# Optimization experiments

Measured on AMD Instinct MI355X. Metric: run time of the kernel, lower is better.

Reference implementation:

```python
import jax, jax.numpy as jnp
import numpy as np

UNITS = 64
NUM_LEVELS = 4
ORDER = 4  # order=-1 defaults to num_levels
NUM_FEATURES = 64  # 63 input features + 1 time channel
LEN_TENSORS = NUM_LEVELS * (NUM_LEVELS + 1) // 2  # 10


def setup_inputs() -> dict:
    key = jax.random.key(0)
    k1, k2 = jax.random.split(key)
    X = jax.random.normal(k1, (32, 2048, 63), dtype=jnp.float32)
    # learned low-rank kernel [num_features, len_tensors, units]; small scale keeps
    # higher-level signature products numerically tame
    kernel = jax.random.normal(k2, (NUM_FEATURES, LEN_TENSORS, UNITS), dtype=jnp.float32) * 0.02
    return {"X": X, "kernel": kernel}


def _ecumsum(x):
    # exclusive cumulative sum along time axis (axis=1), forward direction
    return jnp.cumsum(x, axis=1) - x


def reference(X, kernel):
    B, T, _ = X.shape
    # add_time=True: linear time channel in [-1, 1]
    t = jnp.arange(T, dtype=X.dtype) * (2.0 / (T - 1.0)) - 1.0
    time = jnp.broadcast_to(t[None, :, None], (B, T, 1))
    Xa = jnp.concatenate([time, X], axis=-1)  # [B, T, F]
    # low-rank projection: [B, T, len_tensors, units]
    M = jnp.einsum('btf,fku->btku', Xa, kernel)
    # difference=True: forward increments, zero-padded at t=0
    M = jnp.concatenate([jnp.zeros_like(M[:, :1]), M[:, 1:] - M[:, :-1]], axis=1)

    # level 1
    out = jnp.sum(M[..., 0, :], axis=1)  # [B, units]

    k = 1
    for m in range(1, NUM_LEVELS):
        R = [M[..., k, :]]  # list of [B, T, units]
        k += 1
        for i in range(1, m + 1):
            d = min(i + 1, ORDER)
            A = sum(R)
            Mk = M[..., k, :]
            R_next = [Mk * _ecumsum(A)]
            for j in range(1, d):
                R_next.append(Mk * R[j - 1] / jnp.asarray(j + 1, dtype=X.dtype))
            k += 1
            R = R_next
        out = out + jnp.sum(sum(R), axis=1)
    return out
```

## Files before the change

kernel.cpp:

```cpp
#include <hip/hip_runtime.h>


#define TT 2048
#define NFX 63
#define KT 10
#define NU 64
#define NQ 17
#define NCC 32
#define NSEG 4

#define MAPS_BYTES (32u * NCC * NQ * NU * 4u)
#define PLANE      40960u

typedef __attribute__((ext_vector_type(16))) float f32x16v;
typedef __attribute__((ext_vector_type(8)))  short bf16x8v;

enum {Qo=0, Qa1, Qa3, QaA, Qa6, QaP, QaQ, Qd1, Qd3, QdA, Qd6, QdP, QdQ,
      QtA3, QtP6, QtQP, QtQ6};

__device__ __forceinline__ unsigned short bf16_rne(float x) {
  unsigned int u = __float_as_uint(x);
  unsigned int r = (u + 0x7FFFu + ((u >> 16) & 1u)) >> 16;
  return (unsigned short)r;
}
__device__ __forceinline__ float bf16f(unsigned short h) {
  return __uint_as_float(((unsigned int)h) << 16);
}

__device__ __forceinline__ void compose_maps(const float* q1, const float* q2,
                                             float* r)
{
  r[Qo]  = q1[Qo] + q2[Qo]
         + q2[Qa1]*q1[Qd1] + q2[Qa3]*q1[Qd3] + q2[QaA]*q1[QdA]
         + q2[Qa6]*q1[Qd6] + q2[QaP]*q1[QdP] + q2[QaQ]*q1[QdQ];
  r[Qa1] = q1[Qa1] + q2[Qa1];
  r[Qa3] = q1[Qa3] + q2[Qa3] + q1[QtA3]*q2[QaA];
  r[QaA] = q1[QaA] + q2[QaA];
  r[Qa6] = q1[Qa6] + q2[Qa6] + q1[QtP6]*q2[QaP] + q1[QtQ6]*q2[QaQ];
  r[QaP] = q1[QaP] + q2[QaP] + q1[QtQP]*q2[QaQ];
  r[QaQ] = q1[QaQ] + q2[QaQ];
  r[Qd1] = q1[Qd1] + q2[Qd1];
  r[Qd3] = q1[Qd3] + q2[Qd3];
  r[QdA] = q1[QdA] + q2[QdA] + q2[QtA3]*q1[Qd3];
  r[Qd6] = q1[Qd6] + q2[Qd6];
  r[QdP] = q1[QdP] + q2[QdP] + q2[QtP6]*q1[Qd6];
  r[QdQ] = q1[QdQ] + q2[QdQ] + q2[QtQP]*q1[QdP] + q2[QtQ6]*q1[Qd6];
  r[QtA3] = q1[QtA3] + q2[QtA3];
  r[QtP6] = q1[QtP6] + q2[QtP6];
  r[QtQP] = q1[QtQP] + q2[QtQP];
  r[QtQ6] = q1[QtQ6] + q2[QtQ6] + q2[QtQP]*q1[QtP6];
}

__global__ __launch_bounds__(256)
void lrsig_prep_kernel(const float* __restrict__ Kw,
                       unsigned short* __restrict__ kwb)
{
  int e = blockIdx.x * 256 + threadIdx.x;
  int j  = e & 7;
  int l  = (e >> 3) & 63;
  int ks = (e >> 9) & 3;
  int ub = (e >> 11) & 1;
  int nt = e >> 12;
  int f = ks * 16 + (l >> 5) * 8 + j;
  int u = ub * 32 + (l & 31);
  float x = Kw[(f * KT + nt) * NU + u];
  unsigned short hi = bf16_rne(x);
  unsigned short lo = bf16_rne(x - bf16f(hi));
  kwb[e] = hi;
  kwb[PLANE + e] = lo;
}

#define LOADB(S) do {                                                        \
  _Pragma("unroll")                                                          \
  for (int ks = 0; ks < 4; ++ks) {                                           \
    const unsigned short* bp = kwb + ((((S) * 2 + ub) * 4 + ks) * 512) + l*8;\
    bh[ks] = *(const bf16x8v*)(bp);                                          \
    bl[ks] = *(const bf16x8v*)(bp + PLANE);                                  \
  } } while (0)

#define MFMA12(ACC) do {                                                     \
  _Pragma("unroll")                                                          \
  for (int ks = 0; ks < 4; ++ks) {                                           \
    ACC = __builtin_amdgcn_mfma_f32_32x32x16_bf16(ah[ks], bh[ks], ACC, 0,0,0); \
    ACC = __builtin_amdgcn_mfma_f32_32x32x16_bf16(al[ks], bh[ks], ACC, 0,0,0); \
    ACC = __builtin_amdgcn_mfma_f32_32x32x16_bf16(ah[ks], bl[ks], ACC, 0,0,0); \
  } } while (0)

#define ZERO(ACC) do { _Pragma("unroll")                                     \
  for (int zi = 0; zi < 16; ++zi) ACC[zi] = 0.f; } while (0)

__global__ __launch_bounds__(256)
void lrsig_chunk_kernel(const float* __restrict__ X,
                        const unsigned short* __restrict__ kwb,
                        float* __restrict__ wmaps)
{
  __shared__ __align__(16) float smemf[8192];
  char* smem = (char*)smemf;
  float* rawf = smemf + 4096;

  const int b   = blockIdx.y;
  const int c   = blockIdx.x;
  const int tid = threadIdx.x;
  const int l   = tid & 63;
  const int w   = tid >> 6;
  const int rt  = w >> 1;
  const int ub  = w & 1;
  const int col = l & 31;
  const int hi8 = l >> 5;
  const int t0  = c * 64;

  float sv[16];
  {
    const float* Xb = X + (size_t)b * TT * NFX;
    const int base = (t0 - 1) * NFX;
#pragma unroll
    for (int ii = 0; ii < 16; ++ii) {
      int i = tid + ii * 256;
      int off = base + i + ((c == 0 && i < NFX) ? NFX : 0);
      sv[ii] = (i < 65 * NFX) ? Xb[off] : 0.f;
    }
  }

  bf16x8v bh[4], bl[4];
  LOADB(0);

#pragma unroll
  for (int ii = 0; ii < 16; ++ii) {
    int i = tid + ii * 256;
    if (i < 65 * NFX) rawf[i] = sv[ii];
  }
  __syncthreads();

  {
    float v0[16], v1[16];
#pragma unroll
    for (int ii = 0; ii < 16; ++ii) {
      int e = tid + ii * 256;
      if (e < 64 * NFX) { v0[ii] = rawf[e]; v1[ii] = rawf[e + NFX]; }
    }
#pragma unroll
    for (int ii = 0; ii < 16; ++ii) {
      int e = tid + ii * 256;
      if (e < 64 * NFX) {
        int r2 = e / NFX;
        int c2 = e - r2 * NFX;
        float d = v1[ii] - v0[ii];
        unsigned short h  = bf16_rne(d);
        unsigned short lo = bf16_rne(d - bf16f(h));
        int byte = r2 * 128 + ((2 * (c2 + 1)) ^ ((r2 & 7) << 4));
        *(unsigned short*)(smem + byte)        = h;
        *(unsigned short*)(smem + 8192 + byte) = lo;
      }
    }
  }
  if (tid < 64) {
    int r2 = tid;
    float d = (t0 + r2 == 0) ? 0.f : (2.0f / 2047.0f);
    unsigned short h  = bf16_rne(d);
    unsigned short lo = bf16_rne(d - bf16f(h));
    int byte = r2 * 128 + ((0) ^ ((r2 & 7) << 4));
    *(unsigned short*)(smem + byte)        = h;
    *(unsigned short*)(smem + 8192 + byte) = lo;
  }
  __syncthreads();

  const int row = rt * 32 + col;
  const int colbase = ub * 32 + col;

  bf16x8v ah[4], al[4];
#pragma unroll
  for (int ks = 0; ks < 4; ++ks) {
    const int f0 = ks * 16 + hi8 * 8;
    const int abyte = row * 128 + ((2 * f0) ^ ((row & 7) << 4));
    ah[ks] = *(const bf16x8v*)(smem + abyte);
    al[ks] = *(const bf16x8v*)(smem + 8192 + abyte);
  }

  float Ao[4], Aa1[4], Ad1[4];
  float Ba3[4], BaA[4], Bd3[4], BdA[4], BtA3[4];

  {
    f32x16v accA[3];
    ZERO(accA[0]); ZERO(accA[1]); ZERO(accA[2]);
    MFMA12(accA[0]); LOADB(1);
    MFMA12(accA[1]); LOADB(2);
    MFMA12(accA[2]); LOADB(3);
#pragma unroll
    for (int j = 0; j < 4; ++j) {
      float o = 0.f, a1 = 0.f, lc1 = 0.f;
#pragma unroll
      for (int i = 0; i < 4; ++i) {
        const int r = 4 * j + i;
        float m0 = accA[0][r], m1 = accA[1][r], m2 = accA[2][r];
        o   += m0 + m2 * (lc1 + 0.5f * m1);
        a1  += m2;
        lc1 += m1;
      }
      Ao[j] = o; Aa1[j] = a1; Ad1[j] = lc1;
    }
  }

  {
    f32x16v accB[3];
    ZERO(accB[0]); ZERO(accB[1]); ZERO(accB[2]);
    MFMA12(accB[0]); LOADB(4);
    MFMA12(accB[1]); LOADB(5);
    MFMA12(accB[2]); LOADB(6);
#pragma unroll
    for (int j = 0; j < 4; ++j) {
      float o = 0.f, a3 = 0.f, aA = 0.f, lc3 = 0.f, lcA = 0.f, g4 = 0.f;
#pragma unroll
      for (int i = 0; i < 4; ++i) {
        const int r = 4 * j + i;
        float m3 = accB[0][r], m4 = accB[1][r], m5 = accB[2][r];
        float s0 = m4 * lc3;
        float s1 = 0.5f * m4 * m3;
        o   += m5 * (lcA + 0.5f * s0 + (1.f/3.f) * s1);
        a3  += m5 * (g4 + 0.5f * m4);
        aA  += m5;
        lcA += s0 + s1;
        g4  += m4;
        lc3 += m3;
      }
      Ao[j] += o;
      Ba3[j] = a3; BaA[j] = aA; Bd3[j] = lc3; BdA[j] = lcA; BtA3[j] = g4;
    }
  }

  float tot[NQ];
  {
    f32x16v accC[4];
    ZERO(accC[0]); ZERO(accC[1]); ZERO(accC[2]); ZERO(accC[3]);
    MFMA12(accC[0]); LOADB(7);
    MFMA12(accC[1]); LOADB(8);
    MFMA12(accC[2]); LOADB(9);
    MFMA12(accC[3]);

#pragma unroll
    for (int j = 0; j < 4; ++j) {
      float o = 0.f, a6 = 0.f, aP = 0.f, aQ = 0.f;
      float lc6 = 0.f, lcP = 0.f, lcQ = 0.f, g7 = 0.f, g8 = 0.f, hh = 0.f;
#pragma unroll
      for (int i = 0; i < 4; ++i) {
        const int r = 4 * j + i;
        float m6 = accC[0][r], m7 = accC[1][r], m8 = accC[2][r], m9 = accC[3][r];
        float p0 = m7 * lc6;
        float p1 = 0.5f * m7 * m6;
        float q0 = m8 * lcP;
        float q1 = 0.5f * m8 * p0;
        float q2 = (1.f/3.f) * m8 * p1;
        o   += m9 * (lcQ + 0.5f * q0 + (1.f/3.f) * q1 + 0.25f * q2);
        a6  += m9 * (hh + m8 * (0.5f * g7 + (1.f/6.f) * m7));
        aP  += m9 * (g8 + 0.5f * m8);
        aQ  += m9;
        hh  += m8 * (g7 + 0.5f * m7);
        lcP += p0 + p1;
        lcQ += q0 + q1 + q2;
        g7 += m7; g8 += m8; lc6 += m6;
      }
      float mj[NQ];
      mj[Qo] = Ao[j] + o;
      mj[Qa1] = Aa1[j]; mj[Qa3] = Ba3[j]; mj[QaA] = BaA[j];
      mj[Qa6] = a6;     mj[QaP] = aP;     mj[QaQ] = aQ;
      mj[Qd1] = Ad1[j]; mj[Qd3] = Bd3[j]; mj[QdA] = BdA[j];
      mj[Qd6] = lc6;    mj[QdP] = lcP;    mj[QdQ] = lcQ;
      mj[QtA3] = BtA3[j]; mj[QtP6] = g7;  mj[QtQP] = g8; mj[QtQ6] = hh;

      float q1v[NQ], q2v[NQ], m8r[NQ];
#pragma unroll
      for (int q = 0; q < NQ; ++q) {
        float oth = __shfl_xor(mj[q], 32);
        q1v[q] = hi8 ? oth : mj[q];
        q2v[q] = hi8 ? mj[q] : oth;
      }
      compose_maps(q1v, q2v, m8r);

      if (j == 0) {
#pragma unroll
        for (int q = 0; q < NQ; ++q) tot[q] = m8r[q];
      } else {
        float nt_[NQ];
        compose_maps(tot, m8r, nt_);
#pragma unroll
        for (int q = 0; q < NQ; ++q) tot[q] = nt_[q];
      }
    }
  }

  if (hi8 == 0) {
    float* p = &rawf[(rt * NQ) * NU + colbase];
#pragma unroll
    for (int q = 0; q < NQ; ++q) p[q * NU] = tot[q];
  }
  __syncthreads();

  if (tid < NU) {
    const int uu = tid;
    float q1v[NQ], q2v[NQ], rv[NQ];
#pragma unroll
    for (int q = 0; q < NQ; ++q) {
      q1v[q] = rawf[(0 * NQ + q) * NU + uu];
      q2v[q] = rawf[(1 * NQ + q) * NU + uu];
    }
    compose_maps(q1v, q2v, rv);
    float* p = &wmaps[(((size_t)b * NCC + c) * NQ) * NU + uu];
#pragma unroll
    for (int q = 0; q < NQ; ++q) p[q * NU] = rv[q];
  }
}

__global__ __launch_bounds__(256)
void lrsig_combine_kernel(const float* __restrict__ wmaps,
                          float* __restrict__ out)
{
  __shared__ float sm[NSEG * NQ * NU];
  const int b   = blockIdx.x;
  const int seg = threadIdx.x >> 6;
  const int u   = threadIdx.x & 63;

  float tot[NQ];
  {
    const float* p0 = &wmaps[(((size_t)b * NCC + seg * 8) * NQ) * NU + u];
#pragma unroll
    for (int q = 0; q < NQ; ++q) tot[q] = p0[q * NU];
  }
  for (int i = 1; i < 8; ++i) {
    const float* p = &wmaps[(((size_t)b * NCC + seg * 8 + i) * NQ) * NU + u];
    float m[NQ], r[NQ];
#pragma unroll
    for (int q = 0; q < NQ; ++q) m[q] = p[q * NU];
    compose_maps(tot, m, r);
#pragma unroll
    for (int q = 0; q < NQ; ++q) tot[q] = r[q];
  }
#pragma unroll
  for (int q = 0; q < NQ; ++q) sm[(seg * NQ + q) * NU + u] = tot[q];
  __syncthreads();

  if (threadIdx.x < NU) {
    const int uu = threadIdx.x;
    float c1 = 0.f, c3 = 0.f, cA = 0.f, c6 = 0.f, cP = 0.f, cQ = 0.f, o = 0.f;
#pragma unroll
    for (int s = 0; s < NSEG; ++s) {
      float q[NQ];
#pragma unroll
      for (int i = 0; i < NQ; ++i) q[i] = sm[(s * NQ + i) * NU + uu];
      o  += q[0] + q[1]*c1 + q[2]*c3 + q[3]*cA + q[4]*c6 + q[5]*cP + q[6]*cQ;
      cA += q[13]*c3 + q[9];
      cQ += q[15]*cP + q[16]*c6 + q[12];
      cP += q[14]*c6 + q[11];
      c1 += q[7]; c3 += q[8]; c6 += q[10];
    }
    out[b * 64 + uu] = o;
  }
}

extern "C" void kernel_launch(void* const* d_in, const int* in_sizes, int n_in,
                              void* d_out, int out_size, void* d_ws, size_t ws_size,
                              hipStream_t stream) {
  const float* X  = (const float*)d_in[0];
  const float* Kw = (const float*)d_in[1];
  float* out = (float*)d_out;
  float* wmaps = (float*)d_ws;
  unsigned short* kwb = (unsigned short*)((char*)d_ws + MAPS_BYTES);

  hipLaunchKernelGGL(lrsig_prep_kernel, dim3(160), dim3(256), 0, stream,
                     Kw, kwb);
  hipLaunchKernelGGL(lrsig_chunk_kernel, dim3(NCC, 32), dim3(256), 0, stream,
                     X, kwb, wmaps);
  hipLaunchKernelGGL(lrsig_combine_kernel, dim3(32), dim3(256), 0, stream,
                     wmaps, out);
}
```

Before: 48.43 us.

## Split chunk kernel work across two wave groups by independent signature components

Doubles the chunk kernel's block to 512 threads and assigns half the waves to levels 1-2 (six projection slices) and half to level 3 (four slices). The 17-entry combined map is split into two independent maps of 8 and 10 entries with separate compose routines, stored as 18 entries per chunk. This shortens the serial MFMA and scan chain per wave and shrinks per-thread register state, at the cost of larger blocks and an imbalanced split (six versus four slices).

```diff
diff --git a/kernel.cpp b/kernel.cpp
--- a/kernel.cpp
+++ b/kernel.cpp
@@ -5,18 +5,16 @@
 #define NFX 63
 #define KT 10
 #define NU 64
-#define NQ 17
+#define NQS 18
 #define NCC 32
 #define NSEG 4
 
-#define MAPS_BYTES (32u * NCC * NQ * NU * 4u)
+#define MAPS_BYTES (32u * NCC * NQS * NU * 4u)
 #define PLANE      40960u
 
 typedef __attribute__((ext_vector_type(16))) float f32x16v;
 typedef __attribute__((ext_vector_type(8)))  short bf16x8v;
 
-enum {Qo=0, Qa1, Qa3, QaA, Qa6, QaP, QaQ, Qd1, Qd3, QdA, Qd6, QdP, QdQ,
-      QtA3, QtP6, QtQP, QtQ6};
 
 __device__ __forceinline__ unsigned short bf16_rne(float x) {
   unsigned int u = __float_as_uint(x);
@@ -27,28 +25,32 @@
   return __uint_as_float(((unsigned int)h) << 16);
 }
 
-__device__ __forceinline__ void compose_maps(const float* q1, const float* q2,
-                                             float* r)
-{
-  r[Qo]  = q1[Qo] + q2[Qo]
-         + q2[Qa1]*q1[Qd1] + q2[Qa3]*q1[Qd3] + q2[QaA]*q1[QdA]
-         + q2[Qa6]*q1[Qd6] + q2[QaP]*q1[QdP] + q2[QaQ]*q1[QdQ];
-  r[Qa1] = q1[Qa1] + q2[Qa1];
-  r[Qa3] = q1[Qa3] + q2[Qa3] + q1[QtA3]*q2[QaA];
-  r[QaA] = q1[QaA] + q2[QaA];
-  r[Qa6] = q1[Qa6] + q2[Qa6] + q1[QtP6]*q2[QaP] + q1[QtQ6]*q2[QaQ];
-  r[QaP] = q1[QaP] + q2[QaP] + q1[QtQP]*q2[QaQ];
-  r[QaQ] = q1[QaQ] + q2[QaQ];
-  r[Qd1] = q1[Qd1] + q2[Qd1];
-  r[Qd3] = q1[Qd3] + q2[Qd3];
-  r[QdA] = q1[QdA] + q2[QdA] + q2[QtA3]*q1[Qd3];
-  r[Qd6] = q1[Qd6] + q2[Qd6];
-  r[QdP] = q1[QdP] + q2[QdP] + q2[QtP6]*q1[Qd6];
-  r[QdQ] = q1[QdQ] + q2[QdQ] + q2[QtQP]*q1[QdP] + q2[QtQ6]*q1[Qd6];
-  r[QtA3] = q1[QtA3] + q2[QtA3];
-  r[QtP6] = q1[QtP6] + q2[QtP6];
-  r[QtQP] = q1[QtQP] + q2[QtQP];
-  r[QtQ6] = q1[QtQ6] + q2[QtQ6] + q2[QtQP]*q1[QtP6];
+__device__ __forceinline__ void compose_ab(const float* q1, const float* q2,
+                                           float* r)
+{
+  r[0] = q1[0] + q2[0] + q2[1]*q1[4] + q2[2]*q1[5] + q2[3]*q1[6];
+  r[1] = q1[1] + q2[1];
+  r[2] = q1[2] + q2[2] + q1[7]*q2[3];
+  r[3] = q1[3] + q2[3];
+  r[4] = q1[4] + q2[4];
+  r[5] = q1[5] + q2[5];
+  r[6] = q1[6] + q2[6] + q2[7]*q1[5];
+  r[7] = q1[7] + q2[7];
+}
+
+__device__ __forceinline__ void compose_c(const float* q1, const float* q2,
+                                          float* r)
+{
+  r[0] = q1[0] + q2[0] + q2[1]*q1[4] + q2[2]*q1[5] + q2[3]*q1[6];
+  r[1] = q1[1] + q2[1] + q1[7]*q2[2] + q1[9]*q2[3];
+  r[2] = q1[2] + q2[2] + q1[8]*q2[3];
+  r[3] = q1[3] + q2[3];
+  r[4] = q1[4] + q2[4];
+  r[5] = q1[5] + q2[5] + q2[7]*q1[4];
+  r[6] = q1[6] + q2[6] + q2[8]*q1[5] + q2[9]*q1[4];
+  r[7] = q1[7] + q2[7];
+  r[8] = q1[8] + q2[8];
+  r[9] = q1[9] + q2[9] + q2[8]*q1[7];
 }
 
 __global__ __launch_bounds__(256)
@@ -89,7 +91,7 @@
 #define ZERO(ACC) do { _Pragma("unroll")                                     \
   for (int zi = 0; zi < 16; ++zi) ACC[zi] = 0.f; } while (0)
 
-__global__ __launch_bounds__(256)
+__global__ __launch_bounds__(512)
 void lrsig_chunk_kernel(const float* __restrict__ X,
                         const unsigned short* __restrict__ kwb,
                         float* __restrict__ wmaps)
@@ -103,44 +105,45 @@
   const int tid = threadIdx.x;
   const int l   = tid & 63;
   const int w   = tid >> 6;
-  const int rt  = w >> 1;
-  const int ub  = w & 1;
+  const int cg  = w & 1;
+  const int ub  = (w >> 1) & 1;
+  const int rt  = w >> 2;
   const int col = l & 31;
   const int hi8 = l >> 5;
   const int t0  = c * 64;
 
-  float sv[16];
+  float sv[8];
   {
     const float* Xb = X + (size_t)b * TT * NFX;
     const int base = (t0 - 1) * NFX;
 #pragma unroll
-    for (int ii = 0; ii < 16; ++ii) {
-      int i = tid + ii * 256;
+    for (int ii = 0; ii < 8; ++ii) {
+      int i = tid + ii * 512;
       int off = base + i + ((c == 0 && i < NFX) ? NFX : 0);
       sv[ii] = (i < 65 * NFX) ? Xb[off] : 0.f;
     }
   }
 
   bf16x8v bh[4], bl[4];
-  LOADB(0);
-
-#pragma unroll
-  for (int ii = 0; ii < 16; ++ii) {
-    int i = tid + ii * 256;
+  LOADB(cg ? 6 : 0);
+
+#pragma unroll
+  for (int ii = 0; ii < 8; ++ii) {
+    int i = tid + ii * 512;
     if (i < 65 * NFX) rawf[i] = sv[ii];
   }
   __syncthreads();
 
   {
-    float v0[16], v1[16];
-#pragma unroll
-    for (int ii = 0; ii < 16; ++ii) {
-      int e = tid + ii * 256;
+    float v0[8], v1[8];
+#pragma unroll
+    for (int ii = 0; ii < 8; ++ii) {
+      int e = tid + ii * 512;
       if (e < 64 * NFX) { v0[ii] = rawf[e]; v1[ii] = rawf[e + NFX]; }
     }
 #pragma unroll
-    for (int ii = 0; ii < 16; ++ii) {
-      int e = tid + ii * 256;
+    for (int ii = 0; ii < 8; ++ii) {
+      int e = tid + ii * 512;
       if (e < 64 * NFX) {
         int r2 = e / NFX;
         int c2 = e - r2 * NFX;
@@ -176,66 +179,72 @@
     al[ks] = *(const bf16x8v*)(smem + 8192 + abyte);
   }
 
-  float Ao[4], Aa1[4], Ad1[4];
-  float Ba3[4], BaA[4], Bd3[4], BdA[4], BtA3[4];
-
-  {
-    f32x16v accA[3];
-    ZERO(accA[0]); ZERO(accA[1]); ZERO(accA[2]);
-    MFMA12(accA[0]); LOADB(1);
-    MFMA12(accA[1]); LOADB(2);
-    MFMA12(accA[2]); LOADB(3);
+  if (cg == 0) {
+    f32x16v acc[6];
+    ZERO(acc[0]); ZERO(acc[1]); ZERO(acc[2]);
+    ZERO(acc[3]); ZERO(acc[4]); ZERO(acc[5]);
+    MFMA12(acc[0]); LOADB(1);
+    MFMA12(acc[1]); LOADB(2);
+    MFMA12(acc[2]); LOADB(3);
+    MFMA12(acc[3]); LOADB(4);
+    MFMA12(acc[4]); LOADB(5);
+    MFMA12(acc[5]);
+
+    float tot[8];
 #pragma unroll
     for (int j = 0; j < 4; ++j) {
-      float o = 0.f, a1 = 0.f, lc1 = 0.f;
+      float oA = 0.f, a1 = 0.f, lc1 = 0.f;
+      float oB = 0.f, a3 = 0.f, aA = 0.f, lc3 = 0.f, lcA = 0.f, g4 = 0.f;
 #pragma unroll
       for (int i = 0; i < 4; ++i) {
         const int r = 4 * j + i;
-        float m0 = accA[0][r], m1 = accA[1][r], m2 = accA[2][r];
-        o   += m0 + m2 * (lc1 + 0.5f * m1);
+        float m0 = acc[0][r], m1 = acc[1][r], m2 = acc[2][r];
+        float m3 = acc[3][r], m4 = acc[4][r], m5 = acc[5][r];
+        oA  += m0 + m2 * (lc1 + 0.5f * m1);
         a1  += m2;
         lc1 += m1;
-      }
-      Ao[j] = o; Aa1[j] = a1; Ad1[j] = lc1;
-    }
-  }
-
-  {
-    f32x16v accB[3];
-    ZERO(accB[0]); ZERO(accB[1]); ZERO(accB[2]);
-    MFMA12(accB[0]); LOADB(4);
-    MFMA12(accB[1]); LOADB(5);
-    MFMA12(accB[2]); LOADB(6);
-#pragma unroll
-    for (int j = 0; j < 4; ++j) {
-      float o = 0.f, a3 = 0.f, aA = 0.f, lc3 = 0.f, lcA = 0.f, g4 = 0.f;
-#pragma unroll
-      for (int i = 0; i < 4; ++i) {
-        const int r = 4 * j + i;
-        float m3 = accB[0][r], m4 = accB[1][r], m5 = accB[2][r];
         float s0 = m4 * lc3;
         float s1 = 0.5f * m4 * m3;
-        o   += m5 * (lcA + 0.5f * s0 + (1.f/3.f) * s1);
+        oB  += m5 * (lcA + 0.5f * s0 + (1.f/3.f) * s1);
         a3  += m5 * (g4 + 0.5f * m4);
         aA  += m5;
         lcA += s0 + s1;
         g4  += m4;
         lc3 += m3;
       }
-      Ao[j] += o;
-      Ba3[j] = a3; BaA[j] = aA; Bd3[j] = lc3; BdA[j] = lcA; BtA3[j] = g4;
-    }
-  }
-
-  float tot[NQ];
-  {
-    f32x16v accC[4];
-    ZERO(accC[0]); ZERO(accC[1]); ZERO(accC[2]); ZERO(accC[3]);
-    MFMA12(accC[0]); LOADB(7);
-    MFMA12(accC[1]); LOADB(8);
-    MFMA12(accC[2]); LOADB(9);
-    MFMA12(accC[3]);
-
+      float pm[8] = {oA + oB, a1, a3, aA, lc1, lc3, lcA, g4};
+      float q1v[8], q2v[8], m8r[8];
+#pragma unroll
+      for (int q = 0; q < 8; ++q) {
+        float oth = __shfl_xor(pm[q], 32);
+        q1v[q] = hi8 ? oth : pm[q];
+        q2v[q] = hi8 ? pm[q] : oth;
+      }
+      compose_ab(q1v, q2v, m8r);
+      if (j == 0) {
+#pragma unroll
+        for (int q = 0; q < 8; ++q) tot[q] = m8r[q];
+      } else {
+        float nx[8];
+        compose_ab(tot, m8r, nx);
+#pragma unroll
+        for (int q = 0; q < 8; ++q) tot[q] = nx[q];
+      }
+    }
+    if (hi8 == 0) {
+      float* p = &rawf[(rt * NQS) * NU + colbase];
+#pragma unroll
+      for (int q = 0; q < 8; ++q) p[q * NU] = tot[q];
+    }
+  } else {
+    f32x16v acc[4];
+    ZERO(acc[0]); ZERO(acc[1]); ZERO(acc[2]); ZERO(acc[3]);
+    MFMA12(acc[0]); LOADB(7);
+    MFMA12(acc[1]); LOADB(8);
+    MFMA12(acc[2]); LOADB(9);
+    MFMA12(acc[3]);
+
+    float tot[10];
 #pragma unroll
     for (int j = 0; j < 4; ++j) {
       float o = 0.f, a6 = 0.f, aP = 0.f, aQ = 0.f;
@@ -243,7 +252,7 @@
 #pragma unroll
       for (int i = 0; i < 4; ++i) {
         const int r = 4 * j + i;
-        float m6 = accC[0][r], m7 = accC[1][r], m8 = accC[2][r], m9 = accC[3][r];
+        float m6 = acc[0][r], m7 = acc[1][r], m8 = acc[2][r], m9 = acc[3][r];
         float p0 = m7 * lc6;
         float p1 = 0.5f * m7 * m6;
         float q0 = m8 * lcP;
@@ -258,54 +267,57 @@
         lcQ += q0 + q1 + q2;
         g7 += m7; g8 += m8; lc6 += m6;
       }
-      float mj[NQ];
-      mj[Qo] = Ao[j] + o;
-      mj[Qa1] = Aa1[j]; mj[Qa3] = Ba3[j]; mj[QaA] = BaA[j];
-      mj[Qa6] = a6;     mj[QaP] = aP;     mj[QaQ] = aQ;
-      mj[Qd1] = Ad1[j]; mj[Qd3] = Bd3[j]; mj[QdA] = BdA[j];
-      mj[Qd6] = lc6;    mj[QdP] = lcP;    mj[QdQ] = lcQ;
-      mj[QtA3] = BtA3[j]; mj[QtP6] = g7;  mj[QtQP] = g8; mj[QtQ6] = hh;
-
-      float q1v[NQ], q2v[NQ], m8r[NQ];
-#pragma unroll
-      for (int q = 0; q < NQ; ++q) {
-        float oth = __shfl_xor(mj[q], 32);
-        q1v[q] = hi8 ? oth : mj[q];
-        q2v[q] = hi8 ? mj[q] : oth;
-      }
-      compose_maps(q1v, q2v, m8r);
-
+      float pm[10] = {o, a6, aP, aQ, lc6, lcP, lcQ, g7, g8, hh};
+      float q1v[10], q2v[10], m8r[10];
+#pragma unroll
+      for (int q = 0; q < 10; ++q) {
+        float oth = __shfl_xor(pm[q], 32);
+        q1v[q] = hi8 ? oth : pm[q];
+        q2v[q] = hi8 ? pm[q] : oth;
+      }
+      compose_c(q1v, q2v, m8r);
       if (j == 0) {
 #pragma unroll
-        for (int q = 0; q < NQ; ++q) tot[q] = m8r[q];
+        for (int q = 0; q < 10; ++q) tot[q] = m8r[q];
       } else {
-        float nt_[NQ];
-        compose_maps(tot, m8r, nt_);
-#pragma unroll
-        for (int q = 0; q < NQ; ++q) tot[q] = nt_[q];
-      }
-    }
-  }
-
-  if (hi8 == 0) {
-    float* p = &rawf[(rt * NQ) * NU + colbase];
-#pragma unroll
-    for (int q = 0; q < NQ; ++q) p[q * NU] = tot[q];
+        float nx[10];
+        compose_c(tot, m8r, nx);
+#pragma unroll
+        for (int q = 0; q < 10; ++q) tot[q] = nx[q];
+      }
+    }
+    if (hi8 == 0) {
+      float* p = &rawf[(rt * NQS + 8) * NU + colbase];
+#pragma unroll
+      for (int q = 0; q < 10; ++q) p[q * NU] = tot[q];
+    }
   }
   __syncthreads();
 
   if (tid < NU) {
     const int uu = tid;
-    float q1v[NQ], q2v[NQ], rv[NQ];
-#pragma unroll
-    for (int q = 0; q < NQ; ++q) {
-      q1v[q] = rawf[(0 * NQ + q) * NU + uu];
-      q2v[q] = rawf[(1 * NQ + q) * NU + uu];
-    }
-    compose_maps(q1v, q2v, rv);
-    float* p = &wmaps[(((size_t)b * NCC + c) * NQ) * NU + uu];
-#pragma unroll
-    for (int q = 0; q < NQ; ++q) p[q * NU] = rv[q];
+    float q1v[8], q2v[8], rv[8];
+#pragma unroll
+    for (int q = 0; q < 8; ++q) {
+      q1v[q] = rawf[(0 * NQS + q) * NU + uu];
+      q2v[q] = rawf[(1 * NQS + q) * NU + uu];
+    }
+    compose_ab(q1v, q2v, rv);
+    float* p = &wmaps[(((size_t)b * NCC + c) * NQS) * NU + uu];
+#pragma unroll
+    for (int q = 0; q < 8; ++q) p[q * NU] = rv[q];
+  } else if (tid < 2 * NU) {
+    const int uu = tid - NU;
+    float q1v[10], q2v[10], rv[10];
+#pragma unroll
+    for (int q = 0; q < 10; ++q) {
+      q1v[q] = rawf[(0 * NQS + 8 + q) * NU + uu];
+      q2v[q] = rawf[(1 * NQS + 8 + q) * NU + uu];
+    }
+    compose_c(q1v, q2v, rv);
+    float* p = &wmaps[(((size_t)b * NCC + c) * NQS + 8) * NU + uu];
+#pragma unroll
+    for (int q = 0; q < 10; ++q) p[q * NU] = rv[q];
   }
 }
 
@@ -313,28 +325,37 @@
 void lrsig_combine_kernel(const float* __restrict__ wmaps,
                           float* __restrict__ out)
 {
-  __shared__ float sm[NSEG * NQ * NU];
+  __shared__ float sm[NSEG * NQS * NU];
   const int b   = blockIdx.x;
   const int seg = threadIdx.x >> 6;
   const int u   = threadIdx.x & 63;
 
-  float tot[NQ];
+  float tab[8], tc[10];
   {
-    const float* p0 = &wmaps[(((size_t)b * NCC + seg * 8) * NQ) * NU + u];
-#pragma unroll
-    for (int q = 0; q < NQ; ++q) tot[q] = p0[q * NU];
+    const float* p0 = &wmaps[(((size_t)b * NCC + seg * 8) * NQS) * NU + u];
+#pragma unroll
+    for (int q = 0; q < 8; ++q)  tab[q] = p0[q * NU];
+#pragma unroll
+    for (int q = 0; q < 10; ++q) tc[q]  = p0[(8 + q) * NU];
   }
   for (int i = 1; i < 8; ++i) {
-    const float* p = &wmaps[(((size_t)b * NCC + seg * 8 + i) * NQ) * NU + u];
-    float m[NQ], r[NQ];
-#pragma unroll
-    for (int q = 0; q < NQ; ++q) m[q] = p[q * NU];
-    compose_maps(tot, m, r);
-#pragma unroll
-    for (int q = 0; q < NQ; ++q) tot[q] = r[q];
-  }
-#pragma unroll
-  for (int q = 0; q < NQ; ++q) sm[(seg * NQ + q) * NU + u] = tot[q];
+    const float* p = &wmaps[(((size_t)b * NCC + seg * 8 + i) * NQS) * NU + u];
+    float mab[8], mc[10], rab[8], rc[10];
+#pragma unroll
+    for (int q = 0; q < 8; ++q)  mab[q] = p[q * NU];
+#pragma unroll
+    for (int q = 0; q < 10; ++q) mc[q]  = p[(8 + q) * NU];
+    compose_ab(tab, mab, rab);
+    compose_c(tc, mc, rc);
+#pragma unroll
+    for (int q = 0; q < 8; ++q)  tab[q] = rab[q];
+#pragma unroll
+    for (int q = 0; q < 10; ++q) tc[q]  = rc[q];
+  }
+#pragma unroll
+  for (int q = 0; q < 8; ++q)  sm[(seg * NQS + q) * NU + u]     = tab[q];
+#pragma unroll
+  for (int q = 0; q < 10; ++q) sm[(seg * NQS + 8 + q) * NU + u] = tc[q];
   __syncthreads();
 
   if (threadIdx.x < NU) {
@@ -342,14 +363,15 @@
     float c1 = 0.f, c3 = 0.f, cA = 0.f, c6 = 0.f, cP = 0.f, cQ = 0.f, o = 0.f;
 #pragma unroll
     for (int s = 0; s < NSEG; ++s) {
-      float q[NQ];
-#pragma unroll
-      for (int i = 0; i < NQ; ++i) q[i] = sm[(s * NQ + i) * NU + uu];
-      o  += q[0] + q[1]*c1 + q[2]*c3 + q[3]*cA + q[4]*c6 + q[5]*cP + q[6]*cQ;
-      cA += q[13]*c3 + q[9];
-      cQ += q[15]*cP + q[16]*c6 + q[12];
-      cP += q[14]*c6 + q[11];
-      c1 += q[7]; c3 += q[8]; c6 += q[10];
+      float q[NQS];
+#pragma unroll
+      for (int i = 0; i < NQS; ++i) q[i] = sm[(s * NQS + i) * NU + uu];
+      o  += q[0] + q[8] + q[1]*c1 + q[2]*c3 + q[3]*cA
+          + q[9]*c6 + q[10]*cP + q[11]*cQ;
+      cA += q[7]*c3 + q[6];
+      cQ += q[16]*cP + q[17]*c6 + q[14];
+      cP += q[15]*c6 + q[13];
+      c1 += q[4]; c3 += q[5]; c6 += q[12];
     }
     out[b * 64 + uu] = o;
   }
@@ -366,7 +388,7 @@
 
   hipLaunchKernelGGL(lrsig_prep_kernel, dim3(160), dim3(256), 0, stream,
                      Kw, kwb);
-  hipLaunchKernelGGL(lrsig_chunk_kernel, dim3(NCC, 32), dim3(256), 0, stream,
+  hipLaunchKernelGGL(lrsig_chunk_kernel, dim3(NCC, 32), dim3(512), 0, stream,
                      X, kwb, wmaps);
   hipLaunchKernelGGL(lrsig_combine_kernel, dim3(32), dim3(256), 0, stream,
                      wmaps, out);
```

Result: faster. 42.10 us (-13.1%).
